# Kernel optimization log

Measured on AMD Instinct MI355X. Metric: run time of the kernel, lower is better.

The kernel has to match this reference:

```python
import jax, jax.numpy as jnp
import numpy as np

N, D, H, L, E, OUT, G = 2048, 128, 8, 8, 65536, 64, 16
HD = D // H            # head_dim = 16
SCALE = HD ** -0.5
EPS = 1e-5             # BatchNorm1d eps


def _batchnorm(x, gamma, beta):
    # training-mode BatchNorm1d: biased batch stats over the node axis
    m = jnp.mean(x, axis=0)
    v = jnp.var(x, axis=0)
    return gamma * (x - m) * jax.lax.rsqrt(v + EPS) + beta


def _forward(X, pos_enc, proj_W, proj_b, pe_W, pe_b,
             Wq, bq, Wk, bk, Wv, bv, Wo, bo,
             g1, beta1, W1, b1, W2, b2, g2, beta2,
             mlp_W1, mlp_b1, mlp_W2, mlp_b2,
             edge_index, graph_ids, num_graphs):
    n = X.shape[0]
    # dense adjacency; sparse_coo_tensor sums duplicate edges -> scatter-add
    A = jnp.zeros((n, n), jnp.float32).at[edge_index[0], edge_index[1]].add(1.0)
    h = X @ proj_W + proj_b + pos_enc @ pe_W + pe_b          # [N, D]
    for l in range(L):
        h1 = h
        # NOTE: faithful to torch: [N,D] row-major reshaped to [H,N,HD]
        q = (h @ Wq[l] + bq[l]).reshape(H, n, HD) * SCALE
        k = (h @ Wk[l] + bk[l]).reshape(H, n, HD)
        v = (h @ Wv[l] + bv[l]).reshape(H, n, HD)
        t = jnp.einsum('hnd,hmd->hnm', q, k)                 # [H,N,N]
        attn = jax.nn.softmax(t * A, axis=2)                 # multiply-mask, softmax over all N
        o = jnp.einsum('hnm,hmd->hnd', attn, v).reshape(n, D)
        h = _batchnorm(o @ Wo[l] + bo[l] + h1, g1[l], beta1[l])
        h2 = h
        h = jax.nn.relu(h @ W1[l] + b1[l]) @ W2[l] + b2[l]
        h = _batchnorm(h2 + h, g2[l], beta2[l])
    # SumNode: per-graph node sum
    pooled = jax.ops.segment_sum(h, graph_ids, num_segments=num_graphs)  # [G, D]
    return jax.nn.relu(pooled @ mlp_W1 + mlp_b1) @ mlp_W2 + mlp_b2       # [G, OUT]


def setup_inputs() -> dict:
    key = jax.random.key(0)
    ks = jax.random.split(key, 32)
    f = jnp.float32
    s = D ** -0.5
    inp = {
        'X': jax.random.normal(ks[0], (N, 4), f),
        'pos_enc': jax.random.normal(ks[1], (N, 2), f),
        'edge_index': jax.random.randint(ks[2], (2, E), 0, N),
        'graph_ids': jnp.sort(jax.random.randint(ks[3], (N,), 0, G)).astype(jnp.int32),
        'num_graphs': G,
        'proj_W': jax.random.normal(ks[4], (4, D), f) * 0.5,
        'proj_b': jnp.zeros((D,), f),
        'pe_W': jax.random.normal(ks[5], (2, D), f) * 0.5,
        'pe_b': jnp.zeros((D,), f),
        'Wq': jax.random.normal(ks[6], (L, D, D), f) * s,
        'bq': jnp.zeros((L, D), f),
        'Wk': jax.random.normal(ks[7], (L, D, D), f) * s,
        'bk': jnp.zeros((L, D), f),
        'Wv': jax.random.normal(ks[8], (L, D, D), f) * s,
        'bv': jnp.zeros((L, D), f),
        'Wo': jax.random.normal(ks[9], (L, D, D), f) * s,
        'bo': jnp.zeros((L, D), f),
        'g1': jnp.ones((L, D), f),
        'beta1': jnp.zeros((L, D), f),
        'W1': jax.random.normal(ks[10], (L, D, 2 * D), f) * s,
        'b1': jnp.zeros((L, 2 * D), f),
        'W2': jax.random.normal(ks[11], (L, 2 * D, D), f) * (2 * D) ** -0.5,
        'b2': jnp.zeros((L, D), f),
        'g2': jnp.ones((L, D), f),
        'beta2': jnp.zeros((L, D), f),
        'mlp_W1': jax.random.normal(ks[12], (D, D), f) * s,
        'mlp_b1': jnp.zeros((D,), f),
        'mlp_W2': jax.random.normal(ks[13], (D, OUT), f) * s,
        'mlp_b2': jnp.zeros((OUT,), f),
    }
    return inp


def reference(X, pos_enc, edge_index, graph_ids, num_graphs,
              proj_W, proj_b, pe_W, pe_b,
              Wq, bq, Wk, bk, Wv, bv, Wo, bo,
              g1, beta1, W1, b1, W2, b2, g2, beta2,
              mlp_W1, mlp_b1, mlp_W2, mlp_b2):
    return _forward(X, pos_enc, proj_W, proj_b, pe_W, pe_b,
                    Wq, bq, Wk, bk, Wv, bv, Wo, bo,
                    g1, beta1, W1, b1, W2, b2, g2, beta2,
                    mlp_W1, mlp_b1, mlp_W2, mlp_b2,
                    edge_index, graph_ids, num_graphs)
```

## Files before the change

### kernel.cpp

```cpp
#include <hip/hip_runtime.h>
#include <hip/hip_bf16.h>

#define NN 2048
#define DD 128
#define HH 8
#define HDIM 16
#define LL 8
#define GG 16
#define BNEPS 1e-5f

typedef unsigned int u32;
typedef unsigned long long u64;
typedef __attribute__((ext_vector_type(8))) short bf16x8;
typedef __attribute__((ext_vector_type(8))) unsigned short us8;
typedef __attribute__((ext_vector_type(4))) float f32x4;

__device__ __forceinline__ unsigned short f2bf(float f) {
    union { float f; u32 u; } v; v.f = f;
    u32 u = v.u;
    u32 r = (u + 0x7fffu + ((u >> 16) & 1u)) >> 16;
    return (unsigned short)r;
}

__device__ __forceinline__ float bf2f(unsigned short b) {
    union { u32 u; float f; } v; v.u = ((u32)b) << 16;
    return v.f;
}

__global__ __launch_bounds__(256) void zero_k(uint4* __restrict__ p) {
    p[blockIdx.x * 256 + threadIdx.x] = make_uint4(0u, 0u, 0u, 0u);
}

__global__ __launch_bounds__(256) void scatter_k(const int* __restrict__ ei, u32* __restrict__ A,
                                                 u32* __restrict__ deg, int E) {
    int e = blockIdx.x * 256 + threadIdx.x;
    if (e < E) {
        int s = ei[e];
        int d = ei[E + e];
        u32 old = atomicAdd(&A[s * NN + d], 1u);
        if (old == 0u) atomicAdd(&deg[s], 1u);
    }
}

__global__ __launch_bounds__(256) void scan_k(const u32* __restrict__ deg, u32* __restrict__ rowptr) {
    __shared__ u32 part[256];
    int t = threadIdx.x;
    u32 loc[8]; u32 s = 0;
#pragma unroll
    for (int i = 0; i < 8; i++) { loc[i] = deg[t * 8 + i]; s += loc[i]; }
    part[t] = s; __syncthreads();
    for (int off = 1; off < 256; off <<= 1) {
        u32 vprev = (t >= off) ? part[t - off] : 0u;
        __syncthreads();
        part[t] += vprev;
        __syncthreads();
    }
    u32 run = (t == 0) ? 0u : part[t - 1];
    if (t == 0) rowptr[0] = 0u;
#pragma unroll
    for (int i = 0; i < 8; i++) { run += loc[i]; rowptr[t * 8 + i + 1] = run; }
}

__global__ __launch_bounds__(256) void emit_k(const u32* __restrict__ A, const u32* __restrict__ rowptr,
                                              u32* __restrict__ colidx, u32* __restrict__ cntv) {
    int r = blockIdx.x, tid = threadIdx.x;
    int lane = tid & 63, wid = tid >> 6;
    __shared__ u32 wsum[4];
    u32 base = rowptr[r];
    u32 cb = 0;
    for (int c0 = 0; c0 < NN; c0 += 256) {
        int c = c0 + tid;
        u32 a = A[r * NN + c];
        bool p = (a != 0u);
        u64 bal = __ballot(p);
        u32 rankw = (u32)__popcll(bal & ((1ull << lane) - 1ull));
        if (lane == 0) wsum[wid] = (u32)__popcll(bal);
        __syncthreads();
        u32 woff = 0;
#pragma unroll
        for (int w2 = 0; w2 < 4; w2++) if (w2 < wid) woff += wsum[w2];
        u32 tot = wsum[0] + wsum[1] + wsum[2] + wsum[3];
        if (p) { u32 pos = base + cb + woff + rankw; colidx[pos] = (u32)c; cntv[pos] = a; }
        cb += tot;
        __syncthreads();
    }
}

__global__ __launch_bounds__(256) void wconv_k(const float* __restrict__ Wq, const float* __restrict__ Wk,
                                               const float* __restrict__ Wv, const float* __restrict__ Wo,
                                               const float* __restrict__ W1, const float* __restrict__ W2,
                                               us8* __restrict__ Wf) {
    int tid = blockIdx.x * 256 + threadIdx.x;
    int layer = tid >> 14;
    int r = tid & 16383;
    const float* src;
    int s, NT, ld;
    if (r < 8192) {
        int reg = r >> 11;
        s = r & 2047;
        NT = 8; ld = 128;
        const float* bases[4] = {Wq, Wk, Wv, Wo};
        src = bases[reg] + layer * 16384;
    } else if (r < 12288) {
        s = r - 8192;
        NT = 16; ld = 256;
        src = W1 + layer * 32768;
    } else {
        s = r - 12288;
        NT = 8; ld = 128;
        src = W2 + layer * 32768;
    }
    int lane = s & 63;
    int t = s >> 6;
    int nt = t % NT;
    int kt = t / NT;
    int col = nt * 16 + (lane & 15);
    int k0 = kt * 32 + (lane >> 4) * 8;
    us8 o;
#pragma unroll
    for (int j = 0; j < 8; j++) o[j] = f2bf(src[(k0 + j) * ld + col]);
    Wf[tid] = o;
}

__global__ __launch_bounds__(256) void h0_k(const float* __restrict__ X, const float* __restrict__ pe,
                                            const float* __restrict__ pW, const float* __restrict__ pb,
                                            const float* __restrict__ peW, const float* __restrict__ peb,
                                            float* __restrict__ h) {
    int idx = blockIdx.x * 256 + threadIdx.x;
    int r = idx >> 7, d = idx & 127;
    float acc = pb[d] + peb[d];
    acc += X[r * 4 + 0] * pW[0 * DD + d];
    acc += X[r * 4 + 1] * pW[1 * DD + d];
    acc += X[r * 4 + 2] * pW[2 * DD + d];
    acc += X[r * 4 + 3] * pW[3 * DD + d];
    acc += pe[r * 2 + 0] * peW[0 * DD + d];
    acc += pe[r * 2 + 1] * peW[1 * DD + d];
    h[idx] = acc;
}

__device__ __forceinline__ void finalize_stats2(const float* __restrict__ ps, const float* __restrict__ pss,
                                                const float* __restrict__ gamma, const float* __restrict__ beta,
                                                float* aS, float* cS, float* sred, int tidx) {
    if (ps) {
        int d = tidx & 127, half = tidx >> 7;
        float s = 0.f, s2 = 0.f;
        const float* p0 = ps + half * 64 * 128 + d;
        const float* p1 = pss + half * 64 * 128 + d;
#pragma unroll 8
        for (int i = 0; i < 64; i++) { s += p0[i * 128]; s2 += p1[i * 128]; }
        sred[tidx] = s;
        sred[256 + tidx] = s2;
        __syncthreads();
        if (tidx < 128) {
            float st = sred[tidx] + sred[tidx + 128];
            float s2t = sred[256 + tidx] + sred[256 + tidx + 128];
            float mean = st * (1.0f / NN);
            float var = s2t * (1.0f / NN) - mean * mean;
            float rstd = rsqrtf(var + BNEPS);
            float a = gamma[tidx] * rstd;
            aS[tidx] = a;
            cS[tidx] = beta[tidx] - mean * a;
        }
    } else if (tidx < 128) {
        aS[tidx] = 1.f;
        cS[tidx] = 0.f;
    }
}

__global__ __launch_bounds__(256) void qkv_k(const float* __restrict__ t,
                                             const float* __restrict__ ps, const float* __restrict__ pss,
                                             const float* __restrict__ gamma, const float* __restrict__ beta,
                                             const bf16x8* __restrict__ Wfl,
                                             const float* __restrict__ bq, const float* __restrict__ bk,
                                             const float* __restrict__ bv,
                                             float* __restrict__ q, unsigned short* __restrict__ k,
                                             unsigned short* __restrict__ v,
                                             float* __restrict__ psv) {
    __shared__ float aS[128], cS[128], sred[512];
    int tidx = threadIdx.x;
    finalize_stats2(ps, pss, gamma, beta, aS, cS, sred, tidx);
    __syncthreads();
    int strip = blockIdx.x;
    int m0 = strip * 16;
    int lane = tidx & 63, wv = tidx >> 6;
    int arow = m0 + (lane & 15);
    int k0b = (lane >> 4) * 8;
    bf16x8 af[4];
#pragma unroll
    for (int kt = 0; kt < 4; kt++) {
        int k0 = kt * 32 + k0b;
        const float* tp = t + arow * DD + k0;
        float4 v0 = *(const float4*)(tp);
        float4 v1 = *(const float4*)(tp + 4);
        float vals[8] = {v0.x, v0.y, v0.z, v0.w, v1.x, v1.y, v1.z, v1.w};
        bf16x8 f;
#pragma unroll
        for (int j = 0; j < 8; j++) f[j] = (short)f2bf(vals[j] * aS[k0 + j] + cS[k0 + j]);
        af[kt] = f;
    }
#pragma unroll
    for (int ti = 0; ti < 6; ti++) {
        int tile = wv * 6 + ti;
        int mat = tile >> 3, nt = tile & 7;
        const bf16x8* wb = Wfl + mat * 2048;
        f32x4 acc = {0.f, 0.f, 0.f, 0.f};
#pragma unroll
        for (int kt = 0; kt < 4; kt++)
            acc = __builtin_amdgcn_mfma_f32_16x16x32_bf16(af[kt], wb[(kt * 8 + nt) * 64 + lane], acc, 0, 0, 0);
        int col = nt * 16 + (lane & 15);
        int r0 = m0 + (lane >> 4) * 4;
        if (mat == 0) {
            float bb = bq[col];
#pragma unroll
            for (int j = 0; j < 4; j++) q[(r0 + j) * DD + col] = (acc[j] + bb) * 0.25f;
        } else {
            const float* bias = (mat == 1) ? bk : bv;
            unsigned short* outp = (mat == 1) ? k : v;
            float bb = bias[col];
            unsigned short rb[4];
            float rounded[4];
#pragma unroll
            for (int j = 0; j < 4; j++) {
                rb[j] = f2bf(acc[j] + bb);
                rounded[j] = bf2f(rb[j]);
                outp[(r0 + j) * DD + col] = rb[j];
            }
            if (mat == 2) {
                float cs = rounded[0] + rounded[1] + rounded[2] + rounded[3];
                cs += __shfl_xor(cs, 16);
                cs += __shfl_xor(cs, 32);
                if (lane < 16) psv[strip * 128 + col] = cs;
            }
        }
    }
}

__global__ __launch_bounds__(256) void attn2_k(const float* __restrict__ q, const unsigned short* __restrict__ kb,
                                               const unsigned short* __restrict__ vb, const u32* __restrict__ rowptr,
                                               const u32* __restrict__ colidx, const u32* __restrict__ cntv,
                                               const float* __restrict__ psv, unsigned short* __restrict__ obb) {
    int tid = threadIdx.x;
    int bid = blockIdx.x;
    int hh = bid >> 7;
    __shared__ float vred[16][17];
    __shared__ float vsS[16];
    {
        int d = tid & 15, part = tid >> 4;
        int strip = hh * 16 + part;
        float s = 0.f;
#pragma unroll
        for (int i = 0; i < 8; i++) s += psv[strip * 128 + i * 16 + d];
        vred[d][part] = s;
    }
    __syncthreads();
    if (tid < 16) {
        float s = 0.f;
#pragma unroll
        for (int i = 0; i < 16; i++) s += vred[tid][i];
        vsS[tid] = s;
    }
    __syncthreads();

    int lane = tid & 15;
    int gidx = bid * 16 + (tid >> 4);
    int nn = gidx & (NN - 1);
    const float* qr = q + hh * (NN * HDIM) + nn * HDIM;
    float qv[16];
    *(float4*)&qv[0]  = *(const float4*)(qr + 0);
    *(float4*)&qv[4]  = *(const float4*)(qr + 4);
    *(float4*)&qv[8]  = *(const float4*)(qr + 8);
    *(float4*)&qv[12] = *(const float4*)(qr + 12);
    int rs = (int)rowptr[nn], re = (int)rowptr[nn + 1];
    int deg = re - rs;

    float s[8];
    int mc[8];
    float lm = -1e30f;
#pragma unroll
    for (int ch = 0; ch < 8; ch++) {
        s[ch] = -1e30f; mc[ch] = 0;
        if (ch * 16 < deg) {
            int e = rs + ch * 16 + lane;
            if (e < re) {
                mc[ch] = (int)colidx[e];
                float c = (float)cntv[e];
                const unsigned short* kr = kb + hh * (NN * HDIM) + mc[ch] * HDIM;
                us8 klo = *(const us8*)(kr);
                us8 khi = *(const us8*)(kr + 8);
                float d = 0.f;
#pragma unroll
                for (int i = 0; i < 8; i++) d += qv[i] * bf2f(klo[i]);
#pragma unroll
                for (int i = 0; i < 8; i++) d += qv[i + 8] * bf2f(khi[i]);
                s[ch] = c * d;
            }
            lm = fmaxf(lm, s[ch]);
        }
    }
    for (int base = rs + 128; base < re; base += 16) {
        int e = base + lane;
        if (e < re) {
            int m2 = (int)colidx[e];
            float c = (float)cntv[e];
            const unsigned short* kr = kb + hh * (NN * HDIM) + m2 * HDIM;
            us8 klo = *(const us8*)(kr);
            us8 khi = *(const us8*)(kr + 8);
            float d = 0.f;
#pragma unroll
            for (int i = 0; i < 8; i++) d += qv[i] * bf2f(klo[i]);
#pragma unroll
            for (int i = 0; i < 8; i++) d += qv[i + 8] * bf2f(khi[i]);
            lm = fmaxf(lm, c * d);
        }
    }
#pragma unroll
    for (int off = 1; off < 16; off <<= 1) lm = fmaxf(lm, __shfl_xor(lm, off));
    float rowmax = fmaxf(lm, 0.f);
    float em = __expf(-rowmax);

    float z = 0.f;
    float acc[16];
#pragma unroll
    for (int i = 0; i < 16; i++) acc[i] = 0.f;
#pragma unroll
    for (int ch = 0; ch < 8; ch++) {
        if (ch * 16 < deg) {
            int e = rs + ch * 16 + lane;
            if (e < re) {
                float w = __expf(s[ch] - rowmax);
                z += w;
                float coef = w - em;
                const unsigned short* vr = vb + hh * (NN * HDIM) + mc[ch] * HDIM;
                us8 vlo = *(const us8*)(vr);
                us8 vhi = *(const us8*)(vr + 8);
#pragma unroll
                for (int i = 0; i < 8; i++) acc[i] += coef * bf2f(vlo[i]);
#pragma unroll
                for (int i = 0; i < 8; i++) acc[i + 8] += coef * bf2f(vhi[i]);
            }
        }
    }
    for (int base = rs + 128; base < re; base += 16) {
        int e = base + lane;
        if (e < re) {
            int m2 = (int)colidx[e];
            float c = (float)cntv[e];
            const unsigned short* kr = kb + hh * (NN * HDIM) + m2 * HDIM;
            us8 klo = *(const us8*)(kr);
            us8 khi = *(const us8*)(kr + 8);
            float d = 0.f;
#pragma unroll
            for (int i = 0; i < 8; i++) d += qv[i] * bf2f(klo[i]);
#pragma unroll
            for (int i = 0; i < 8; i++) d += qv[i + 8] * bf2f(khi[i]);
            float w = __expf(c * d - rowmax);
            z += w;
            float coef = w - em;
            const unsigned short* vr = vb + hh * (NN * HDIM) + m2 * HDIM;
            us8 vlo = *(const us8*)(vr);
            us8 vhi = *(const us8*)(vr + 8);
#pragma unroll
            for (int i = 0; i < 8; i++) acc[i] += coef * bf2f(vlo[i]);
#pragma unroll
            for (int i = 0; i < 8; i++) acc[i + 8] += coef * bf2f(vhi[i]);
        }
    }
#pragma unroll
    for (int off = 1; off < 16; off <<= 1) {
        z += __shfl_xor(z, off);
#pragma unroll
        for (int i = 0; i < 16; i++) acc[i] += __shfl_xor(acc[i], off);
    }
    if (lane == 0) {
        float Z = z + (float)(NN - deg) * em;
        float inv = 1.f / Z;
        unsigned short* orow = obb + hh * (NN * HDIM) + nn * HDIM;
        us8 lo, hi;
#pragma unroll
        for (int i = 0; i < 8; i++) {
            lo[i] = f2bf((acc[i] + em * vsS[i]) * inv);
            hi[i] = f2bf((acc[i + 8] + em * vsS[i + 8]) * inv);
        }
        *(us8*)(orow + 0) = lo;
        *(us8*)(orow + 8) = hi;
    }
}

__global__ __launch_bounds__(256) void gemmO_k(const unsigned short* __restrict__ obb,
                                               const bf16x8* __restrict__ Wfo,
                                               const float* __restrict__ bo,
                                               const float* __restrict__ tprev,
                                               const float* __restrict__ ps, const float* __restrict__ pss,
                                               const float* __restrict__ gamma, const float* __restrict__ beta,
                                               float* __restrict__ t1,
                                               float* __restrict__ ps1, float* __restrict__ pss1) {
    __shared__ float aS[128], cS[128], sred[512];
    int tidx = threadIdx.x;
    finalize_stats2(ps, pss, gamma, beta, aS, cS, sred, tidx);
    __syncthreads();
    int strip = blockIdx.x;
    int m0 = strip * 16;
    int lane = tidx & 63, wv = tidx >> 6;
    int arow = m0 + (lane & 15);
    int k0b = (lane >> 4) * 8;
    bf16x8 af[4];
#pragma unroll
    for (int kt = 0; kt < 4; kt++)
        af[kt] = *(const bf16x8*)(obb + arow * DD + kt * 32 + k0b);
#pragma unroll
    for (int ti = 0; ti < 2; ti++) {
        int nt = wv * 2 + ti;
        f32x4 acc = {0.f, 0.f, 0.f, 0.f};
#pragma unroll
        for (int kt = 0; kt < 4; kt++)
            acc = __builtin_amdgcn_mfma_f32_16x16x32_bf16(af[kt], Wfo[(kt * 8 + nt) * 64 + lane], acc, 0, 0, 0);
        int col = nt * 16 + (lane & 15);
        int r0 = m0 + (lane >> 4) * 4;
        float bb = bo[col];
        float a = aS[col], c = cS[col];
        float sum = 0.f, sumsq = 0.f;
#pragma unroll
        for (int j = 0; j < 4; j++) {
            float res = tprev[(r0 + j) * DD + col] * a + c;
            float v0 = acc[j] + bb + res;
            t1[(r0 + j) * DD + col] = v0;
            sum += v0; sumsq += v0 * v0;
        }
        sum += __shfl_xor(sum, 16);  sum += __shfl_xor(sum, 32);
        sumsq += __shfl_xor(sumsq, 16); sumsq += __shfl_xor(sumsq, 32);
        if (lane < 16) { ps1[strip * 128 + col] = sum; pss1[strip * 128 + col] = sumsq; }
    }
}

__global__ __launch_bounds__(256) void mlp_k(const float* __restrict__ t1,
                                             const float* __restrict__ ps1, const float* __restrict__ pss1,
                                             const float* __restrict__ g1, const float* __restrict__ be1,
                                             const bf16x8* __restrict__ Wf1, const float* __restrict__ b1,
                                             const bf16x8* __restrict__ Wf2, const float* __restrict__ b2,
                                             float* __restrict__ t2,
                                             float* __restrict__ ps2, float* __restrict__ pss2) {
    __shared__ float aS[128], cS[128], sred[512];
    __shared__ unsigned short midL[16][264];
    int tidx = threadIdx.x;
    finalize_stats2(ps1, pss1, g1, be1, aS, cS, sred, tidx);
    __syncthreads();
    int strip = blockIdx.x;
    int m0 = strip * 16;
    int lane = tidx & 63, wv = tidx >> 6;
    int lrow = lane & 15;
    int arow = m0 + lrow;
    int k0b = (lane >> 4) * 8;
    bf16x8 af[4];
#pragma unroll
    for (int kt = 0; kt < 4; kt++) {
        int k0 = kt * 32 + k0b;
        const float* tp = t1 + arow * DD + k0;
        float4 v0 = *(const float4*)(tp);
        float4 v1 = *(const float4*)(tp + 4);
        float vals[8] = {v0.x, v0.y, v0.z, v0.w, v1.x, v1.y, v1.z, v1.w};
        bf16x8 f;
#pragma unroll
        for (int j = 0; j < 8; j++) f[j] = (short)f2bf(vals[j] * aS[k0 + j] + cS[k0 + j]);
        af[kt] = f;
    }
#pragma unroll
    for (int ti = 0; ti < 4; ti++) {
        int nt = wv * 4 + ti;
        f32x4 acc = {0.f, 0.f, 0.f, 0.f};
#pragma unroll
        for (int kt = 0; kt < 4; kt++)
            acc = __builtin_amdgcn_mfma_f32_16x16x32_bf16(af[kt], Wf1[(kt * 16 + nt) * 64 + lane], acc, 0, 0, 0);
        int col = nt * 16 + (lane & 15);
        int r0l = (lane >> 4) * 4;
        float bb = b1[col];
#pragma unroll
        for (int j = 0; j < 4; j++)
            midL[r0l + j][col] = f2bf(fmaxf(acc[j] + bb, 0.f));
    }
    __syncthreads();
    bf16x8 af2[8];
#pragma unroll
    for (int kt = 0; kt < 8; kt++)
        af2[kt] = *(const bf16x8*)(&midL[lrow][kt * 32 + k0b]);
#pragma unroll
    for (int ti = 0; ti < 2; ti++) {
        int nt = wv * 2 + ti;
        f32x4 acc = {0.f, 0.f, 0.f, 0.f};
#pragma unroll
        for (int kt = 0; kt < 8; kt++)
            acc = __builtin_amdgcn_mfma_f32_16x16x32_bf16(af2[kt], Wf2[(kt * 8 + nt) * 64 + lane], acc, 0, 0, 0);
        int col = nt * 16 + (lane & 15);
        int r0 = m0 + (lane >> 4) * 4;
        float bb = b2[col];
        float a = aS[col], c = cS[col];
        float sum = 0.f, sumsq = 0.f;
#pragma unroll
        for (int j = 0; j < 4; j++) {
            float res = t1[(r0 + j) * DD + col] * a + c;
            float v0 = acc[j] + bb + res;
            t2[(r0 + j) * DD + col] = v0;
            sum += v0; sumsq += v0 * v0;
        }
        sum += __shfl_xor(sum, 16);  sum += __shfl_xor(sum, 32);
        sumsq += __shfl_xor(sumsq, 16); sumsq += __shfl_xor(sumsq, 32);
        if (lane < 16) { ps2[strip * 128 + col] = sum; pss2[strip * 128 + col] = sumsq; }
    }
}

__global__ __launch_bounds__(256) void pool_head_k(const float* __restrict__ t, const float* __restrict__ ps,
                                                   const float* __restrict__ pss, const float* __restrict__ gamma,
                                                   const float* __restrict__ beta, const int* __restrict__ gid,
                                                   const float* __restrict__ W1, const float* __restrict__ b1,
                                                   const float* __restrict__ W2, const float* __restrict__ b2,
                                                   float* __restrict__ out) {
    __shared__ float aS[128], cS[128], sred[512];
    __shared__ float psum[2][128];
    __shared__ float p[128], midv[128];
    int tidx = threadIdx.x, g = blockIdx.x;
    finalize_stats2(ps, pss, gamma, beta, aS, cS, sred, tidx);
    __syncthreads();
    int lo = 0, hi = NN;
    while (lo < hi) { int mid = (lo + hi) >> 1; if (gid[mid] < g) lo = mid + 1; else hi = mid; }
    int start = lo;
    lo = start; hi = NN;
    while (lo < hi) { int mid = (lo + hi) >> 1; if (gid[mid] <= g) lo = mid + 1; else hi = mid; }
    int end = lo;
    int d = tidx & 127, half = tidx >> 7;
    float acc = 0.f;
    for (int r = start + half; r < end; r += 2) acc += t[r * DD + d] * aS[d] + cS[d];
    psum[half][d] = acc;
    __syncthreads();
    if (tidx < 128) p[tidx] = psum[0][tidx] + psum[1][tidx];
    __syncthreads();
    if (tidx < 128) {
        float a = b1[tidx];
        for (int k2 = 0; k2 < 128; k2++) a += p[k2] * W1[k2 * 128 + tidx];
        midv[tidx] = fmaxf(a, 0.f);
    }
    __syncthreads();
    if (tidx < 64) {
        float a = b2[tidx];
        for (int k2 = 0; k2 < 128; k2++) a += midv[k2] * W2[k2 * 64 + tidx];
        out[g * 64 + tidx] = a;
    }
}

extern "C" void kernel_launch(void* const* d_in, const int* in_sizes, int n_in,
                              void* d_out, int out_size, void* d_ws, size_t ws_size,
                              hipStream_t stream) {
    (void)n_in; (void)out_size; (void)ws_size;
    const float* X      = (const float*)d_in[0];
    const float* pos    = (const float*)d_in[1];
    const int*   ei     = (const int*)d_in[2];
    const int*   gid    = (const int*)d_in[3];
    const float* proj_W = (const float*)d_in[5];
    const float* proj_b = (const float*)d_in[6];
    const float* pe_W   = (const float*)d_in[7];
    const float* pe_b   = (const float*)d_in[8];
    const float* Wq     = (const float*)d_in[9];
    const float* bq     = (const float*)d_in[10];
    const float* Wk     = (const float*)d_in[11];
    const float* bk     = (const float*)d_in[12];
    const float* Wv     = (const float*)d_in[13];
    const float* bv     = (const float*)d_in[14];
    const float* Wo     = (const float*)d_in[15];
    const float* bo     = (const float*)d_in[16];
    const float* g1     = (const float*)d_in[17];
    const float* beta1  = (const float*)d_in[18];
    const float* W1     = (const float*)d_in[19];
    const float* b1     = (const float*)d_in[20];
    const float* W2     = (const float*)d_in[21];
    const float* b2     = (const float*)d_in[22];
    const float* g2     = (const float*)d_in[23];
    const float* beta2  = (const float*)d_in[24];
    const float* mW1    = (const float*)d_in[25];
    const float* mb1    = (const float*)d_in[26];
    const float* mW2    = (const float*)d_in[27];
    const float* mb2    = (const float*)d_in[28];
    float* out = (float*)d_out;

    int E = in_sizes[2] / 2;

    char* w = (char*)d_ws;
    u32*   Adense = (u32*)(w + 0);
    u32*   deg    = (u32*)(w + 16777216);
    u32*   rowptr = (u32*)(w + 16785408);
    u32*   colidx = (u32*)(w + 16793856);
    u32*   cntv   = (u32*)(w + 17056000);
    float* tA     = (float*)(w + 17318144);
    float* tB     = (float*)(w + 18366720);
    float* qb     = (float*)(w + 19415296);
    unsigned short* kb = (unsigned short*)(w + 20463872);
    unsigned short* vb = (unsigned short*)(w + 20988160);
    unsigned short* obb = (unsigned short*)(w + 21512448);
    float* psA    = (float*)(w + 22036736);
    float* pssA   = (float*)(w + 22102272);
    float* psB    = (float*)(w + 22167808);
    float* pssB   = (float*)(w + 22233344);
    float* psv    = (float*)(w + 22298880);
    bf16x8* Wf    = (bf16x8*)(w + 22364416);

    zero_k<<<4098, 256, 0, stream>>>((uint4*)Adense);
    scatter_k<<<(E + 255) / 256, 256, 0, stream>>>(ei, Adense, deg, E);
    scan_k<<<1, 256, 0, stream>>>(deg, rowptr);
    emit_k<<<NN, 256, 0, stream>>>(Adense, rowptr, colidx, cntv);

    wconv_k<<<512, 256, 0, stream>>>(Wq, Wk, Wv, Wo, W1, W2, (us8*)Wf);

    h0_k<<<NN * DD / 256, 256, 0, stream>>>(X, pos, proj_W, proj_b, pe_W, pe_b, tA);

    for (int l = 0; l < LL; l++) {
        const bf16x8* Wfl = Wf + l * 16384;
        const float* psIn  = (l == 0) ? nullptr : psA;
        const float* pssIn = (l == 0) ? nullptr : pssA;
        const float* gIn   = (l == 0) ? nullptr : (g2 + (l - 1) * DD);
        const float* bIn   = (l == 0) ? nullptr : (beta2 + (l - 1) * DD);

        qkv_k<<<128, 256, 0, stream>>>(tA, psIn, pssIn, gIn, bIn, Wfl,
                                       bq + l * DD, bk + l * DD, bv + l * DD, qb, kb, vb, psv);
        attn2_k<<<HH * NN / 16, 256, 0, stream>>>(qb, kb, vb, rowptr, colidx, cntv, psv, obb);
        gemmO_k<<<128, 256, 0, stream>>>(obb, Wfl + 6144, bo + l * DD, tA, psIn, pssIn, gIn, bIn,
                                         tB, psB, pssB);
        mlp_k<<<128, 256, 0, stream>>>(tB, psB, pssB, g1 + l * DD, beta1 + l * DD,
                                       Wfl + 8192, b1 + l * 2 * DD, Wfl + 12288, b2 + l * DD,
                                       tA, psA, pssA);
    }

    pool_head_k<<<GG, 256, 0, stream>>>(tA, psA, pssA, g2 + 7 * DD, beta2 + 7 * DD, gid,
                                        mW1, mb1, mW2, mb2, out);
}
```

Measured before the change: 342.7 us.

## Split QKV, output-projection and MLP GEMMs across more blocks and threads

The QKV kernel now launches three blocks per strip, one per Q/K/V matrix (blockIdx.z), instead of one block doing all 24 tiles. The output-projection kernel is split over two z-blocks, each wave computing one column tile. The MLP kernel uses 512 threads with a four-way stats reduction, and each wave does fewer tiles. The aim is more parallelism on a GPU that was underfilled by 128-block launches, at the cost of redundantly recomputing batchnorm stats and re-reading the input activation strip in every extra block.

```diff
diff --git a/kernel.cpp b/kernel.cpp
--- a/kernel.cpp
+++ b/kernel.cpp
@@ -167,6 +167,35 @@
     }
 }
 
+__device__ __forceinline__ void finalize_stats4(const float* __restrict__ ps, const float* __restrict__ pss,
+                                                const float* __restrict__ gamma, const float* __restrict__ beta,
+                                                float* aS, float* cS, float* sred, int tidx) {
+    if (ps) {
+        int d = tidx & 127, qr = tidx >> 7;
+        float s = 0.f, s2 = 0.f;
+        const float* p0 = ps + qr * 32 * 128 + d;
+        const float* p1 = pss + qr * 32 * 128 + d;
+#pragma unroll 8
+        for (int i = 0; i < 32; i++) { s += p0[i * 128]; s2 += p1[i * 128]; }
+        sred[tidx] = s;
+        sred[512 + tidx] = s2;
+        __syncthreads();
+        if (tidx < 128) {
+            float st = (sred[tidx] + sred[tidx + 128]) + (sred[tidx + 256] + sred[tidx + 384]);
+            float s2t = (sred[512 + tidx] + sred[512 + tidx + 128]) + (sred[512 + tidx + 256] + sred[512 + tidx + 384]);
+            float mean = st * (1.0f / NN);
+            float var = s2t * (1.0f / NN) - mean * mean;
+            float rstd = rsqrtf(var + BNEPS);
+            float a = gamma[tidx] * rstd;
+            aS[tidx] = a;
+            cS[tidx] = beta[tidx] - mean * a;
+        }
+    } else if (tidx < 128) {
+        aS[tidx] = 1.f;
+        cS[tidx] = 0.f;
+    }
+}
+
 __global__ __launch_bounds__(256) void qkv_k(const float* __restrict__ t,
                                              const float* __restrict__ ps, const float* __restrict__ pss,
                                              const float* __restrict__ gamma, const float* __restrict__ beta,
@@ -181,6 +210,7 @@
     finalize_stats2(ps, pss, gamma, beta, aS, cS, sred, tidx);
     __syncthreads();
     int strip = blockIdx.x;
+    int mat = blockIdx.z;
     int m0 = strip * 16;
     int lane = tidx & 63, wv = tidx >> 6;
     int arow = m0 + (lane & 15);
@@ -198,11 +228,10 @@
         for (int j = 0; j < 8; j++) f[j] = (short)f2bf(vals[j] * aS[k0 + j] + cS[k0 + j]);
         af[kt] = f;
     }
-#pragma unroll
-    for (int ti = 0; ti < 6; ti++) {
-        int tile = wv * 6 + ti;
-        int mat = tile >> 3, nt = tile & 7;
-        const bf16x8* wb = Wfl + mat * 2048;
+    const bf16x8* wb = Wfl + mat * 2048;
+#pragma unroll
+    for (int ti = 0; ti < 2; ti++) {
+        int nt = wv * 2 + ti;
         f32x4 acc = {0.f, 0.f, 0.f, 0.f};
 #pragma unroll
         for (int kt = 0; kt < 4; kt++)
@@ -407,9 +436,8 @@
 #pragma unroll
     for (int kt = 0; kt < 4; kt++)
         af[kt] = *(const bf16x8*)(obb + arow * DD + kt * 32 + k0b);
-#pragma unroll
-    for (int ti = 0; ti < 2; ti++) {
-        int nt = wv * 2 + ti;
+    {
+        int nt = blockIdx.z * 4 + wv;
         f32x4 acc = {0.f, 0.f, 0.f, 0.f};
 #pragma unroll
         for (int kt = 0; kt < 4; kt++)
@@ -432,17 +460,17 @@
     }
 }
 
-__global__ __launch_bounds__(256) void mlp_k(const float* __restrict__ t1,
+__global__ __launch_bounds__(512) void mlp_k(const float* __restrict__ t1,
                                              const float* __restrict__ ps1, const float* __restrict__ pss1,
                                              const float* __restrict__ g1, const float* __restrict__ be1,
                                              const bf16x8* __restrict__ Wf1, const float* __restrict__ b1,
                                              const bf16x8* __restrict__ Wf2, const float* __restrict__ b2,
                                              float* __restrict__ t2,
                                              float* __restrict__ ps2, float* __restrict__ pss2) {
-    __shared__ float aS[128], cS[128], sred[512];
+    __shared__ float aS[128], cS[128], sred[1024];
     __shared__ unsigned short midL[16][264];
     int tidx = threadIdx.x;
-    finalize_stats2(ps1, pss1, g1, be1, aS, cS, sred, tidx);
+    finalize_stats4(ps1, pss1, g1, be1, aS, cS, sred, tidx);
     __syncthreads();
     int strip = blockIdx.x;
     int m0 = strip * 16;
@@ -464,8 +492,8 @@
         af[kt] = f;
     }
 #pragma unroll
-    for (int ti = 0; ti < 4; ti++) {
-        int nt = wv * 4 + ti;
+    for (int ti = 0; ti < 2; ti++) {
+        int nt = wv * 2 + ti;
         f32x4 acc = {0.f, 0.f, 0.f, 0.f};
 #pragma unroll
         for (int kt = 0; kt < 4; kt++)
@@ -482,9 +510,8 @@
 #pragma unroll
     for (int kt = 0; kt < 8; kt++)
         af2[kt] = *(const bf16x8*)(&midL[lrow][kt * 32 + k0b]);
-#pragma unroll
-    for (int ti = 0; ti < 2; ti++) {
-        int nt = wv * 2 + ti;
+    {
+        int nt = wv;
         f32x4 acc = {0.f, 0.f, 0.f, 0.f};
 #pragma unroll
         for (int kt = 0; kt < 8; kt++)
@@ -616,12 +643,12 @@
         const float* gIn   = (l == 0) ? nullptr : (g2 + (l - 1) * DD);
         const float* bIn   = (l == 0) ? nullptr : (beta2 + (l - 1) * DD);
 
-        qkv_k<<<128, 256, 0, stream>>>(tA, psIn, pssIn, gIn, bIn, Wfl,
-                                       bq + l * DD, bk + l * DD, bv + l * DD, qb, kb, vb, psv);
+        qkv_k<<<dim3(128, 1, 3), 256, 0, stream>>>(tA, psIn, pssIn, gIn, bIn, Wfl,
+                                                   bq + l * DD, bk + l * DD, bv + l * DD, qb, kb, vb, psv);
         attn2_k<<<HH * NN / 16, 256, 0, stream>>>(qb, kb, vb, rowptr, colidx, cntv, psv, obb);
-        gemmO_k<<<128, 256, 0, stream>>>(obb, Wfl + 6144, bo + l * DD, tA, psIn, pssIn, gIn, bIn,
-                                         tB, psB, pssB);
-        mlp_k<<<128, 256, 0, stream>>>(tB, psB, pssB, g1 + l * DD, beta1 + l * DD,
+        gemmO_k<<<dim3(128, 1, 2), 256, 0, stream>>>(obb, Wfl + 6144, bo + l * DD, tA, psIn, pssIn, gIn, bIn,
+                                                     tB, psB, pssB);
+        mlp_k<<<128, 512, 0, stream>>>(tB, psB, pssB, g1 + l * DD, beta1 + l * DD,
                                        Wfl + 8192, b1 + l * 2 * DD, Wfl + 12288, b2 + l * DD,
                                        tA, psA, pssA);
     }
```

Measured after the change: 313.8 us. 1.09x faster.
